# Performance work log

Hardware: AMD Instinct MI355X
Metric: run time of the kernel (lower is better)

## Reference

```python
import jax, jax.numpy as jnp
import numpy as np

CHUNK = 128
EPS = 1e-12


def causal_prod(q, k, v, chunk=CHUNK):
    """Chunk-parallel causal linear attention numerator and denominator.
    q,k: [B,H,S,D]; v: [B,H,S,E].
    Returns N: [B,H,S,E] = q_n . cumsum_{m<=n}(k_m v_m^T)
            D: [B,H,S]   = q_n . cumsum_{m<=n} k_m
    """
    B, H, S, D = q.shape
    E = v.shape[-1]
    nc = S // chunk
    # [nc, B, H, C, D]
    qc = q.reshape(B, H, nc, chunk, D).transpose(2, 0, 1, 3, 4)
    kc = k.reshape(B, H, nc, chunk, D).transpose(2, 0, 1, 3, 4)
    vc = v.reshape(B, H, nc, chunk, E).transpose(2, 0, 1, 3, 4)
    mask = jnp.tril(jnp.ones((chunk, chunk), dtype=bool))  # j <= i

    def step(carry, xs):
        S_state, Z_state = carry  # [B,H,D,E], [B,H,D]
        qb, kb, vb = xs           # [B,H,C,D], [B,H,C,D], [B,H,C,E]
        scores = jnp.einsum('bhid,bhjd->bhij', qb, kb)
        scores = jnp.where(mask, scores, 0.0)
        # intra-chunk causal part + inter-chunk state part
        Nb = jnp.einsum('bhij,bhje->bhie', scores, vb) \
             + jnp.einsum('bhid,bhde->bhie', qb, S_state)
        Db = scores.sum(-1) + jnp.einsum('bhid,bhd->bhi', qb, Z_state)
        S_state = S_state + jnp.einsum('bhjd,bhje->bhde', kb, vb)
        Z_state = Z_state + kb.sum(axis=2)
        return (S_state, Z_state), (Nb, Db)

    init = (jnp.zeros((B, H, D, E), q.dtype), jnp.zeros((B, H, D), q.dtype))
    _, (N, Dv) = jax.lax.scan(step, init, (qc, kc, vc))
    N = N.transpose(1, 2, 0, 3, 4).reshape(B, H, S, E)
    Dv = Dv.transpose(1, 2, 0, 3).reshape(B, H, S)
    return N, Dv


def setup_inputs() -> dict:
    key = jax.random.key(0)
    k0, k1, k2, k3, k4 = jax.random.split(key, 5)
    B, H, S, D = 2, 8, 4096, 64
    # feature-mapped q/k are positive (softmax random features) -> uniform
    q = jax.random.uniform(k0, (B, H, S, D), dtype=jnp.float32)
    k = jax.random.uniform(k1, (B, H, S, D), dtype=jnp.float32)
    q_rot = jax.random.uniform(k2, (B, H, S, D), dtype=jnp.float32)
    k_rot = jax.random.uniform(k3, (B, H, S, D), dtype=jnp.float32)
    v = jax.random.normal(k4, (B, H, S, D), dtype=jnp.float32)
    return {"q": q, "k": k, "q_rot": q_rot, "k_rot": k_rot, "v": v, "horizon": 512}


def reference(q, k, q_rot, k_rot, v, horizon):
    # causal_linear_attention with local=horizon, rotary branch active
    N1, D1 = causal_prod(q, k, v)
    N2, D2 = causal_prod(q_rot, k_rot, v)
    N = N1 + N2
    Dd = D1 + D2
    local = horizon
    # subtract contribution of keys older than the local window
    ql = q[:, :, local:]
    kl = k[:, :, :-local]
    vl = v[:, :, :-local]
    qrl = q_rot[:, :, local:]
    krl = k_rot[:, :, :-local]
    Ns1, Ds1 = causal_prod(ql, kl, vl)
    Ns2, Ds2 = causal_prod(qrl, krl, vl)
    N = N.at[:, :, local:].add(-(Ns1 + Ns2))
    Dd = Dd.at[:, :, local:].add(-(Ds1 + Ds2))
    out = N * (1.0 / (Dd + EPS))[..., None]
    return out
```

## Files before the change

### kernel.cpp

```cpp
#include <hip/hip_runtime.h>

#define S_LEN 4096
#define Dh 64
#define BQ 128
#define BK 64
#define THREADS 256

typedef __attribute__((ext_vector_type(8))) short bf16x8;
typedef __attribute__((ext_vector_type(4))) float f32x4;

__device__ __forceinline__ short f2bf(float f) {
    union { float f; unsigned u; } c; c.f = f;
    unsigned u = c.u + 0x7FFFu + ((c.u >> 16) & 1u);
    return (short)(u >> 16);
}

__global__ __launch_bounds__(THREADS, 2) void swin_attn(
    const float* __restrict__ q, const float* __restrict__ k,
    const float* __restrict__ qr, const float* __restrict__ kr,
    const float* __restrict__ v, const int* __restrict__ hor,
    float* __restrict__ out)
{
    const int W = hor[0];
    const int q0 = blockIdx.x * BQ;
    const int bh = blockIdx.y;
    const size_t base = (size_t)bh * S_LEN * Dh;

    const int tid = threadIdx.x;
    const int lane = tid & 63;
    const int wv = tid >> 6;
    const int g = lane >> 4;
    const int l16 = lane & 15;

    __shared__ __align__(16) char sK[BK * 256];
    __shared__ __align__(16) char sV[64 * 128];
    __shared__ __align__(16) char sS[4][32 * 128];

    bf16x8 qf[2][4];
    #pragma unroll
    for (int rb = 0; rb < 2; ++rb) {
        int qg = q0 + wv * 32 + rb * 16 + l16;
        const float* qrow  = q  + base + (size_t)qg * Dh;
        const float* qrrow = qr + base + (size_t)qg * Dh;
        #pragma unroll
        for (int fb = 0; fb < 4; ++fb) {
            int feat = fb * 32 + g * 8;
            const float* src = (feat < 64) ? (qrow + feat) : (qrrow + (feat - 64));
            f32x4 a = *(const f32x4*)src;
            f32x4 b = *(const f32x4*)(src + 4);
            bf16x8 fr;
            #pragma unroll
            for (int j = 0; j < 4; ++j) { fr[j] = f2bf(a[j]); fr[4 + j] = f2bf(b[j]); }
            qf[rb][fb] = fr;
        }
    }

    f32x4 nacc[2][4];
    f32x4 dacc[2];
    #pragma unroll
    for (int rb = 0; rb < 2; ++rb) {
        dacc[rb] = (f32x4){0.f, 0.f, 0.f, 0.f};
        #pragma unroll
        for (int eb = 0; eb < 4; ++eb) nacc[rb][eb] = (f32x4){0.f, 0.f, 0.f, 0.f};
    }
    bf16x8 ones;
    #pragma unroll
    for (int j = 0; j < 8; ++j) ones[j] = (short)0x3F80;

    const int lo_key = q0 - (W - 1);
    const int kt_lo = (lo_key <= 0) ? 0 : (lo_key >> 6);
    const int kt_hi = (q0 + BQ - 1) >> 6;

    for (int kt = kt_lo; kt <= kt_hi; ++kt) {
        const int k0 = kt << 6;
        __syncthreads();

        #pragma unroll
        for (int i = 0; i < 4; ++i) {
            int c = tid + THREADS * i;
            int row = c >> 4;
            int f0 = (c & 15) * 8;
            const float* src = (f0 < 64) ? (k  + base + (size_t)(k0 + row) * Dh + f0)
                                         : (kr + base + (size_t)(k0 + row) * Dh + (f0 - 64));
            f32x4 a = *(const f32x4*)src;
            f32x4 b = *(const f32x4*)(src + 4);
            bf16x8 w8;
            #pragma unroll
            for (int j = 0; j < 4; ++j) { w8[j] = f2bf(a[j]); w8[4 + j] = f2bf(b[j]); }
            int off = row * 256 + ((f0 * 2) ^ ((row & 7) << 4));
            *(bf16x8*)(sK + off) = w8;
        }
        #pragma unroll
        for (int i = 0; i < 4; ++i) {
            int c = tid + THREADS * i;
            int row = c >> 4;
            int c4 = (c & 15) * 4;
            f32x4 a = *(const f32x4*)(v + base + (size_t)(k0 + row) * Dh + c4);
            #pragma unroll
            for (int j = 0; j < 4; ++j) {
                int e = c4 + j;
                int off = e * 128 + ((row * 2) ^ ((e & 7) << 4));
                *(short*)(sV + off) = f2bf(a[j]);
            }
        }
        __syncthreads();

        const bool dense = (k0 + BK - 1 <= q0) && (k0 >= q0 + BQ - 1 - (W - 1));

        #pragma unroll
        for (int kb = 0; kb < 4; ++kb) {
            bf16x8 kf[4];
            const int key = kb * 16 + l16;
            const int rowoff = key * 256;
            const int sw = (key & 7) << 4;
            #pragma unroll
            for (int fb = 0; fb < 4; ++fb)
                kf[fb] = *(const bf16x8*)(sK + rowoff + ((fb * 64 + g * 16) ^ sw));
            #pragma unroll
            for (int rb = 0; rb < 2; ++rb) {
                f32x4 s = {0.f, 0.f, 0.f, 0.f};
                #pragma unroll
                for (int fb = 0; fb < 4; ++fb)
                    s = __builtin_amdgcn_mfma_f32_16x16x32_bf16(qf[rb][fb], kf[fb], s, 0, 0, 0);
                const int qrow0 = rb * 16 + g * 4;
                const int qg0 = q0 + wv * 32 + qrow0;
                const int mg = k0 + kb * 16 + l16;
                if (!dense) {
                    #pragma unroll
                    for (int r = 0; r < 4; ++r) {
                        unsigned d = (unsigned)(qg0 + r - mg);
                        if (d >= (unsigned)W) s[r] = 0.f;
                    }
                }
                #pragma unroll
                for (int r = 0; r < 4; ++r) {
                    int row = qrow0 + r;
                    int off = row * 128 + (((kb * 16 + l16) * 2) ^ ((row & 7) << 4));
                    *(short*)(sS[wv] + off) = f2bf(s[r]);
                }
            }
        }

        #pragma unroll
        for (int kb2 = 0; kb2 < 2; ++kb2) {
            bf16x8 af[2];
            #pragma unroll
            for (int rb = 0; rb < 2; ++rb) {
                int row = rb * 16 + l16;
                int off = row * 128 + ((kb2 * 64 + g * 16) ^ ((row & 7) << 4));
                af[rb] = *(const bf16x8*)(sS[wv] + off);
            }
            #pragma unroll
            for (int rb = 0; rb < 2; ++rb)
                dacc[rb] = __builtin_amdgcn_mfma_f32_16x16x32_bf16(af[rb], ones, dacc[rb], 0, 0, 0);
            #pragma unroll
            for (int eb = 0; eb < 4; ++eb) {
                int e = eb * 16 + l16;
                int off = e * 128 + ((kb2 * 64 + g * 16) ^ ((e & 7) << 4));
                bf16x8 bfr = *(const bf16x8*)(sV + off);
                #pragma unroll
                for (int rb = 0; rb < 2; ++rb)
                    nacc[rb][eb] = __builtin_amdgcn_mfma_f32_16x16x32_bf16(af[rb], bfr, nacc[rb][eb], 0, 0, 0);
            }
        }
    }

    #pragma unroll
    for (int rb = 0; rb < 2; ++rb) {
        f32x4 rc;
        #pragma unroll
        for (int r = 0; r < 4; ++r) rc[r] = 1.0f / (dacc[rb][r] + 1e-12f);
        const int qg0 = q0 + wv * 32 + rb * 16 + g * 4;
        #pragma unroll
        for (int eb = 0; eb < 4; ++eb) {
            #pragma unroll
            for (int r = 0; r < 4; ++r) {
                out[base + (size_t)(qg0 + r) * Dh + eb * 16 + l16] = nacc[rb][eb][r] * rc[r];
            }
        }
    }
}

extern "C" void kernel_launch(void* const* d_in, const int* in_sizes, int n_in,
                              void* d_out, int out_size, void* d_ws, size_t ws_size,
                              hipStream_t stream) {
    const float* q  = (const float*)d_in[0];
    const float* k  = (const float*)d_in[1];
    const float* qr = (const float*)d_in[2];
    const float* kr = (const float*)d_in[3];
    const float* v  = (const float*)d_in[4];
    const int* hor  = (const int*)d_in[5];
    float* out = (float*)d_out;

    const int BH = in_sizes[0] / (S_LEN * Dh);
    dim3 grid(S_LEN / BQ, BH);
    hipLaunchKernelGGL(swin_attn, grid, dim3(THREADS), 0, stream,
                       q, k, qr, kr, v, hor, out);
}
```

Measured before the change: 49.89 us.

## Halve query tile, remap grid for XCD locality, coalesce V staging

Shrinks the query block from 128 to 64 rows, with each wave handling 16 query rows instead of 32, and raises the launch-bounds occupancy hint to 4 blocks per CU. The grid becomes one-dimensional with an XCD-aware remap, so that neighbouring query tiles of the same head land on the same XCD and share K/V in its L2. The V transpose into shared memory now has each thread read four rows of one column and do a single 8-byte LDS store, instead of four 2-byte stores. The cost is twice as many blocks, so each K/V tile is loaded and converted more times in total, and there is less MFMA work per K-tile load.

```diff
diff --git a/kernel.cpp b/kernel.cpp
--- a/kernel.cpp
+++ b/kernel.cpp
@@ -2,12 +2,14 @@
 
 #define S_LEN 4096
 #define Dh 64
-#define BQ 128
+#define BQ 64
 #define BK 64
 #define THREADS 256
+#define NXCD 8
 
 typedef __attribute__((ext_vector_type(8))) short bf16x8;
 typedef __attribute__((ext_vector_type(4))) float f32x4;
+typedef __attribute__((ext_vector_type(4))) short bf16x4;
 
 __device__ __forceinline__ short f2bf(float f) {
     union { float f; unsigned u; } c; c.f = f;
@@ -15,15 +17,19 @@
     return (short)(u >> 16);
 }
 
-__global__ __launch_bounds__(THREADS, 2) void swin_attn(
+__global__ __launch_bounds__(THREADS, 4) void swin_attn(
     const float* __restrict__ q, const float* __restrict__ k,
     const float* __restrict__ qr, const float* __restrict__ kr,
     const float* __restrict__ v, const int* __restrict__ hor,
     float* __restrict__ out)
 {
     const int W = hor[0];
-    const int q0 = blockIdx.x * BQ;
-    const int bh = blockIdx.y;
+
+    const int nwg = gridDim.x;
+    const int cpx = nwg >> 3;
+    const int wg = (blockIdx.x & (NXCD - 1)) * cpx + (blockIdx.x >> 3);
+    const int bh = wg >> 6;
+    const int q0 = (wg & 63) * BQ;
     const size_t base = (size_t)bh * S_LEN * Dh;
 
     const int tid = threadIdx.x;
@@ -34,12 +40,11 @@
 
     __shared__ __align__(16) char sK[BK * 256];
     __shared__ __align__(16) char sV[64 * 128];
-    __shared__ __align__(16) char sS[4][32 * 128];
+    __shared__ __align__(16) char sS[4][16 * 128];
 
-    bf16x8 qf[2][4];
-    #pragma unroll
-    for (int rb = 0; rb < 2; ++rb) {
-        int qg = q0 + wv * 32 + rb * 16 + l16;
+    bf16x8 qf[4];
+    {
+        int qg = q0 + wv * 16 + l16;
         const float* qrow  = q  + base + (size_t)qg * Dh;
         const float* qrrow = qr + base + (size_t)qg * Dh;
         #pragma unroll
@@ -51,25 +56,21 @@
             bf16x8 fr;
             #pragma unroll
             for (int j = 0; j < 4; ++j) { fr[j] = f2bf(a[j]); fr[4 + j] = f2bf(b[j]); }
-            qf[rb][fb] = fr;
+            qf[fb] = fr;
         }
     }
 
-    f32x4 nacc[2][4];
-    f32x4 dacc[2];
+    f32x4 nacc[4];
+    f32x4 dacc = (f32x4){0.f, 0.f, 0.f, 0.f};
     #pragma unroll
-    for (int rb = 0; rb < 2; ++rb) {
-        dacc[rb] = (f32x4){0.f, 0.f, 0.f, 0.f};
-        #pragma unroll
-        for (int eb = 0; eb < 4; ++eb) nacc[rb][eb] = (f32x4){0.f, 0.f, 0.f, 0.f};
-    }
+    for (int eb = 0; eb < 4; ++eb) nacc[eb] = (f32x4){0.f, 0.f, 0.f, 0.f};
     bf16x8 ones;
     #pragma unroll
     for (int j = 0; j < 8; ++j) ones[j] = (short)0x3F80;
 
     const int lo_key = q0 - (W - 1);
     const int kt_lo = (lo_key <= 0) ? 0 : (lo_key >> 6);
-    const int kt_hi = (q0 + BQ - 1) >> 6;
+    const int kt_hi = q0 >> 6;
 
     for (int kt = kt_lo; kt <= kt_hi; ++kt) {
         const int k0 = kt << 6;
@@ -93,15 +94,17 @@
         #pragma unroll
         for (int i = 0; i < 4; ++i) {
             int c = tid + THREADS * i;
-            int row = c >> 4;
-            int c4 = (c & 15) * 4;
-            f32x4 a = *(const f32x4*)(v + base + (size_t)(k0 + row) * Dh + c4);
-            #pragma unroll
-            for (int j = 0; j < 4; ++j) {
-                int e = c4 + j;
-                int off = e * 128 + ((row * 2) ^ ((e & 7) << 4));
-                *(short*)(sV + off) = f2bf(a[j]);
-            }
+            int e = c & 63;
+            int k4 = c >> 6;
+            const float* src = v + base + (size_t)(k0 + k4 * 4) * Dh + e;
+            float a0 = src[0];
+            float a1 = src[Dh];
+            float a2 = src[2 * Dh];
+            float a3 = src[3 * Dh];
+            bf16x4 w4;
+            w4[0] = f2bf(a0); w4[1] = f2bf(a1); w4[2] = f2bf(a2); w4[3] = f2bf(a3);
+            int off = e * 128 + ((k4 * 8) ^ ((e & 7) << 4));
+            *(bf16x4*)(sV + off) = w4;
         }
         __syncthreads();
 
@@ -116,67 +119,53 @@
             #pragma unroll
             for (int fb = 0; fb < 4; ++fb)
                 kf[fb] = *(const bf16x8*)(sK + rowoff + ((fb * 64 + g * 16) ^ sw));
+            f32x4 s = {0.f, 0.f, 0.f, 0.f};
             #pragma unroll
-            for (int rb = 0; rb < 2; ++rb) {
-                f32x4 s = {0.f, 0.f, 0.f, 0.f};
-                #pragma unroll
-                for (int fb = 0; fb < 4; ++fb)
-                    s = __builtin_amdgcn_mfma_f32_16x16x32_bf16(qf[rb][fb], kf[fb], s, 0, 0, 0);
-                const int qrow0 = rb * 16 + g * 4;
-                const int qg0 = q0 + wv * 32 + qrow0;
-                const int mg = k0 + kb * 16 + l16;
-                if (!dense) {
-                    #pragma unroll
-                    for (int r = 0; r < 4; ++r) {
-                        unsigned d = (unsigned)(qg0 + r - mg);
-                        if (d >= (unsigned)W) s[r] = 0.f;
-                    }
-                }
+            for (int fb = 0; fb < 4; ++fb)
+                s = __builtin_amdgcn_mfma_f32_16x16x32_bf16(qf[fb], kf[fb], s, 0, 0, 0);
+            const int qrow0 = g * 4;
+            const int qg0 = q0 + wv * 16 + qrow0;
+            const int mg = k0 + kb * 16 + l16;
+            if (!dense) {
                 #pragma unroll
                 for (int r = 0; r < 4; ++r) {
-                    int row = qrow0 + r;
-                    int off = row * 128 + (((kb * 16 + l16) * 2) ^ ((row & 7) << 4));
-                    *(short*)(sS[wv] + off) = f2bf(s[r]);
+                    unsigned d = (unsigned)(qg0 + r - mg);
+                    if (d >= (unsigned)W) s[r] = 0.f;
                 }
+            }
+            #pragma unroll
+            for (int r = 0; r < 4; ++r) {
+                int row = qrow0 + r;
+                int off = row * 128 + (((kb * 16 + l16) * 2) ^ ((row & 7) << 4));
+                *(short*)(sS[wv] + off) = f2bf(s[r]);
             }
         }
 
         #pragma unroll
         for (int kb2 = 0; kb2 < 2; ++kb2) {
-            bf16x8 af[2];
-            #pragma unroll
-            for (int rb = 0; rb < 2; ++rb) {
-                int row = rb * 16 + l16;
-                int off = row * 128 + ((kb2 * 64 + g * 16) ^ ((row & 7) << 4));
-                af[rb] = *(const bf16x8*)(sS[wv] + off);
-            }
-            #pragma unroll
-            for (int rb = 0; rb < 2; ++rb)
-                dacc[rb] = __builtin_amdgcn_mfma_f32_16x16x32_bf16(af[rb], ones, dacc[rb], 0, 0, 0);
+            int arow = l16;
+            int aoff = arow * 128 + ((kb2 * 64 + g * 16) ^ ((arow & 7) << 4));
+            bf16x8 af = *(const bf16x8*)(sS[wv] + aoff);
+            dacc = __builtin_amdgcn_mfma_f32_16x16x32_bf16(af, ones, dacc, 0, 0, 0);
             #pragma unroll
             for (int eb = 0; eb < 4; ++eb) {
                 int e = eb * 16 + l16;
                 int off = e * 128 + ((kb2 * 64 + g * 16) ^ ((e & 7) << 4));
                 bf16x8 bfr = *(const bf16x8*)(sV + off);
-                #pragma unroll
-                for (int rb = 0; rb < 2; ++rb)
-                    nacc[rb][eb] = __builtin_amdgcn_mfma_f32_16x16x32_bf16(af[rb], bfr, nacc[rb][eb], 0, 0, 0);
+                nacc[eb] = __builtin_amdgcn_mfma_f32_16x16x32_bf16(af, bfr, nacc[eb], 0, 0, 0);
             }
         }
     }
 
+    f32x4 rc;
     #pragma unroll
-    for (int rb = 0; rb < 2; ++rb) {
-        f32x4 rc;
+    for (int r = 0; r < 4; ++r) rc[r] = 1.0f / (dacc[r] + 1e-12f);
+    const int qg0 = q0 + wv * 16 + g * 4;
+    #pragma unroll
+    for (int eb = 0; eb < 4; ++eb) {
         #pragma unroll
-        for (int r = 0; r < 4; ++r) rc[r] = 1.0f / (dacc[rb][r] + 1e-12f);
-        const int qg0 = q0 + wv * 32 + rb * 16 + g * 4;
-        #pragma unroll
-        for (int eb = 0; eb < 4; ++eb) {
-            #pragma unroll
-            for (int r = 0; r < 4; ++r) {
-                out[base + (size_t)(qg0 + r) * Dh + eb * 16 + l16] = nacc[rb][eb][r] * rc[r];
-            }
+        for (int r = 0; r < 4; ++r) {
+            out[base + (size_t)(qg0 + r) * Dh + eb * 16 + l16] = nacc[eb][r] * rc[r];
         }
     }
 }
@@ -193,7 +182,7 @@
     float* out = (float*)d_out;
 
     const int BH = in_sizes[0] / (S_LEN * Dh);
-    dim3 grid(S_LEN / BQ, BH);
+    dim3 grid((S_LEN / BQ) * BH);
     hipLaunchKernelGGL(swin_attn, grid, dim3(THREADS), 0, stream,
                        q, k, qr, kr, v, hor, out);
 }
```

After: 58.16 us. 16.6% more time.

## Prepack K/V to swizzled bf16 workspace and double-buffer via global_load_lds

Applied to the files above, without the earlier changes.

Adds a prepack kernel that converts K, K_rot and V once into bf16 tiles in the workspace, already swizzled and with V transposed, so each key tile is converted once instead of once per query block that reads it. The attention kernel then streams these tiles straight into LDS with global_load_lds, double-buffered so the next tile loads while the current one computes. It also remaps block IDs so neighbouring blocks run on related heads. The cost is an extra kernel launch and a workspace round trip. A fallback kernel with vectorised V transposition is used when the workspace is too small.

```diff
diff --git a/kernel.cpp b/kernel.cpp
--- a/kernel.cpp
+++ b/kernel.cpp
@@ -2,12 +2,15 @@
 
 #define S_LEN 4096
 #define Dh 64
-#define BQ 128
-#define BK 64
 #define THREADS 256
+#define KC_TILE 16384
+#define VT_TILE 8192
+#define VT_BASE 16777216ull
+#define WS_NEED 25165824ull
 
 typedef __attribute__((ext_vector_type(8))) short bf16x8;
 typedef __attribute__((ext_vector_type(4))) float f32x4;
+typedef __attribute__((ext_vector_type(4))) short bf16x4;
 
 __device__ __forceinline__ short f2bf(float f) {
     union { float f; unsigned u; } c; c.f = f;
@@ -15,15 +18,62 @@
     return (short)(u >> 16);
 }
 
-__global__ __launch_bounds__(THREADS, 2) void swin_attn(
-    const float* __restrict__ q, const float* __restrict__ k,
-    const float* __restrict__ qr, const float* __restrict__ kr,
-    const float* __restrict__ v, const int* __restrict__ hor,
+__device__ __forceinline__ void gload16(const void* g, void* l) {
+    __builtin_amdgcn_global_load_lds(
+        (const __attribute__((address_space(1))) unsigned int*)g,
+        (__attribute__((address_space(3))) unsigned int*)l, 16, 0, 0);
+}
+
+__global__ __launch_bounds__(THREADS) void prepack(
+    const float* __restrict__ k, const float* __restrict__ kr,
+    const float* __restrict__ v, char* __restrict__ ws)
+{
+    const int t = blockIdx.x * THREADS + threadIdx.x;
+    {
+        const int bh = t >> 16;
+        const int r1 = t & 65535;
+        const int tile = r1 >> 10;
+        const int r2 = r1 & 1023;
+        const int row = r2 >> 4;
+        const int f0 = (r2 & 15) * 8;
+        const size_t rbase = ((size_t)bh * S_LEN + tile * 64 + row) * Dh;
+        const float* src = (f0 < 64) ? (k + rbase + f0) : (kr + rbase + (f0 - 64));
+        f32x4 a = *(const f32x4*)src;
+        f32x4 b = *(const f32x4*)(src + 4);
+        bf16x8 w;
+        #pragma unroll
+        for (int j = 0; j < 4; ++j) { w[j] = f2bf(a[j]); w[4 + j] = f2bf(b[j]); }
+        const int off = row * 256 + ((f0 * 2) ^ ((row & 7) << 4));
+        *(bf16x8*)(ws + (size_t)(bh * 64 + tile) * KC_TILE + off) = w;
+    }
+    {
+        const int bh = t >> 16;
+        const int r1 = t & 65535;
+        const int tile = r1 >> 10;
+        const int r2 = r1 & 1023;
+        const int e = r2 & 63;
+        const int k4 = r2 >> 6;
+        const float* src = v + ((size_t)bh * S_LEN + tile * 64 + k4 * 4) * Dh + e;
+        bf16x4 w;
+        w[0] = f2bf(src[0]);
+        w[1] = f2bf(src[Dh]);
+        w[2] = f2bf(src[2 * Dh]);
+        w[3] = f2bf(src[3 * Dh]);
+        const int off = e * 128 + ((k4 * 8) ^ ((e & 7) << 4));
+        *(bf16x4*)(ws + VT_BASE + (size_t)(bh * 64 + tile) * VT_TILE + off) = w;
+    }
+}
+
+__global__ __launch_bounds__(THREADS, 2) void swin_attn2(
+    const float* __restrict__ q, const float* __restrict__ qr,
+    const char* __restrict__ ws, const int* __restrict__ hor,
     float* __restrict__ out)
 {
     const int W = hor[0];
-    const int q0 = blockIdx.x * BQ;
-    const int bh = blockIdx.y;
+    const int bid = blockIdx.x;
+    const int wg = (bid & 7) * 64 + (bid >> 3);
+    const int bh = wg >> 5;
+    const int q0 = (wg & 31) * 128;
     const size_t base = (size_t)bh * S_LEN * Dh;
 
     const int tid = threadIdx.x;
@@ -32,9 +82,9 @@
     const int g = lane >> 4;
     const int l16 = lane & 15;
 
-    __shared__ __align__(16) char sK[BK * 256];
-    __shared__ __align__(16) char sV[64 * 128];
-    __shared__ __align__(16) char sS[4][32 * 128];
+    __shared__ __align__(16) char sK[2][KC_TILE];
+    __shared__ __align__(16) char sV[2][VT_TILE];
+    __shared__ __align__(16) char sS[4][4096];
 
     bf16x8 qf[2][4];
     #pragma unroll
@@ -69,43 +119,45 @@
 
     const int lo_key = q0 - (W - 1);
     const int kt_lo = (lo_key <= 0) ? 0 : (lo_key >> 6);
-    const int kt_hi = (q0 + BQ - 1) >> 6;
-
+    const int kt_hi = (q0 + 127) >> 6;
+
+    const char* KcB = ws + (size_t)(bh << 6) * KC_TILE;
+    const char* VtB = ws + VT_BASE + (size_t)(bh << 6) * VT_TILE;
+
+    asm volatile("s_waitcnt vmcnt(0)" ::: "memory");
+    __builtin_amdgcn_sched_barrier(0);
+
+#define STAGE(B, KT)                                                              \
+    do {                                                                          \
+        const char* kg_ = KcB + (size_t)(KT) * KC_TILE + wv * 4096 + lane * 16;   \
+        const char* vg_ = VtB + (size_t)(KT) * VT_TILE + wv * 2048 + lane * 16;   \
+        _Pragma("unroll")                                                         \
+        for (int i_ = 0; i_ < 4; ++i_)                                            \
+            gload16(kg_ + i_ * 1024, &sK[B][wv * 4096 + i_ * 1024]);              \
+        _Pragma("unroll")                                                         \
+        for (int i_ = 0; i_ < 2; ++i_)                                            \
+            gload16(vg_ + i_ * 1024, &sV[B][wv * 2048 + i_ * 1024]);              \
+    } while (0)
+
+    STAGE(0, kt_lo);
+
+    int buf = 0;
     for (int kt = kt_lo; kt <= kt_hi; ++kt) {
         const int k0 = kt << 6;
-        __syncthreads();
-
-        #pragma unroll
-        for (int i = 0; i < 4; ++i) {
-            int c = tid + THREADS * i;
-            int row = c >> 4;
-            int f0 = (c & 15) * 8;
-            const float* src = (f0 < 64) ? (k  + base + (size_t)(k0 + row) * Dh + f0)
-                                         : (kr + base + (size_t)(k0 + row) * Dh + (f0 - 64));
-            f32x4 a = *(const f32x4*)src;
-            f32x4 b = *(const f32x4*)(src + 4);
-            bf16x8 w8;
-            #pragma unroll
-            for (int j = 0; j < 4; ++j) { w8[j] = f2bf(a[j]); w8[4 + j] = f2bf(b[j]); }
-            int off = row * 256 + ((f0 * 2) ^ ((row & 7) << 4));
-            *(bf16x8*)(sK + off) = w8;
-        }
-        #pragma unroll
-        for (int i = 0; i < 4; ++i) {
-            int c = tid + THREADS * i;
-            int row = c >> 4;
-            int c4 = (c & 15) * 4;
-            f32x4 a = *(const f32x4*)(v + base + (size_t)(k0 + row) * Dh + c4);
-            #pragma unroll
-            for (int j = 0; j < 4; ++j) {
-                int e = c4 + j;
-                int off = e * 128 + ((row * 2) ^ ((e & 7) << 4));
-                *(short*)(sV + off) = f2bf(a[j]);
-            }
-        }
-        __syncthreads();
-
-        const bool dense = (k0 + BK - 1 <= q0) && (k0 >= q0 + BQ - 1 - (W - 1));
+        const bool more = (kt < kt_hi);
+        if (more) {
+            STAGE(buf ^ 1, kt + 1);
+            asm volatile("s_waitcnt vmcnt(6)" ::: "memory");
+        } else {
+            asm volatile("s_waitcnt vmcnt(0)" ::: "memory");
+        }
+        __builtin_amdgcn_sched_barrier(0);
+        __builtin_amdgcn_s_barrier();
+        asm volatile("" ::: "memory");
+
+        const char* Kb = sK[buf];
+        const char* Vb = sV[buf];
+        const bool dense = (k0 + 63 <= q0) && (k0 >= q0 + 127 - (W - 1));
 
         #pragma unroll
         for (int kb = 0; kb < 4; ++kb) {
@@ -115,7 +167,7 @@
             const int sw = (key & 7) << 4;
             #pragma unroll
             for (int fb = 0; fb < 4; ++fb)
-                kf[fb] = *(const bf16x8*)(sK + rowoff + ((fb * 64 + g * 16) ^ sw));
+                kf[fb] = *(const bf16x8*)(Kb + rowoff + ((fb * 64 + g * 16) ^ sw));
             #pragma unroll
             for (int rb = 0; rb < 2; ++rb) {
                 f32x4 s = {0.f, 0.f, 0.f, 0.f};
@@ -157,6 +209,173 @@
             for (int eb = 0; eb < 4; ++eb) {
                 int e = eb * 16 + l16;
                 int off = e * 128 + ((kb2 * 64 + g * 16) ^ ((e & 7) << 4));
+                bf16x8 bfr = *(const bf16x8*)(Vb + off);
+                #pragma unroll
+                for (int rb = 0; rb < 2; ++rb)
+                    nacc[rb][eb] = __builtin_amdgcn_mfma_f32_16x16x32_bf16(af[rb], bfr, nacc[rb][eb], 0, 0, 0);
+            }
+        }
+
+        asm volatile("" ::: "memory");
+        __builtin_amdgcn_s_barrier();
+        buf ^= 1;
+    }
+#undef STAGE
+
+    #pragma unroll
+    for (int rb = 0; rb < 2; ++rb) {
+        f32x4 rc;
+        #pragma unroll
+        for (int r = 0; r < 4; ++r) rc[r] = 1.0f / (dacc[rb][r] + 1e-12f);
+        const int qg0 = q0 + wv * 32 + rb * 16 + g * 4;
+        #pragma unroll
+        for (int eb = 0; eb < 4; ++eb) {
+            #pragma unroll
+            for (int r = 0; r < 4; ++r) {
+                out[base + (size_t)(qg0 + r) * Dh + eb * 16 + l16] = nacc[rb][eb][r] * rc[r];
+            }
+        }
+    }
+}
+
+__global__ __launch_bounds__(THREADS, 2) void swin_attn_fb(
+    const float* __restrict__ q, const float* __restrict__ k,
+    const float* __restrict__ qr, const float* __restrict__ kr,
+    const float* __restrict__ v, const int* __restrict__ hor,
+    float* __restrict__ out)
+{
+    const int W = hor[0];
+    const int q0 = blockIdx.x * 128;
+    const int bh = blockIdx.y;
+    const size_t base = (size_t)bh * S_LEN * Dh;
+
+    const int tid = threadIdx.x;
+    const int lane = tid & 63;
+    const int wv = tid >> 6;
+    const int g = lane >> 4;
+    const int l16 = lane & 15;
+
+    __shared__ __align__(16) char sK[64 * 256];
+    __shared__ __align__(16) char sV[64 * 128];
+    __shared__ __align__(16) char sS[4][32 * 128];
+
+    bf16x8 qf[2][4];
+    #pragma unroll
+    for (int rb = 0; rb < 2; ++rb) {
+        int qg = q0 + wv * 32 + rb * 16 + l16;
+        const float* qrow  = q  + base + (size_t)qg * Dh;
+        const float* qrrow = qr + base + (size_t)qg * Dh;
+        #pragma unroll
+        for (int fb = 0; fb < 4; ++fb) {
+            int feat = fb * 32 + g * 8;
+            const float* src = (feat < 64) ? (qrow + feat) : (qrrow + (feat - 64));
+            f32x4 a = *(const f32x4*)src;
+            f32x4 b = *(const f32x4*)(src + 4);
+            bf16x8 fr;
+            #pragma unroll
+            for (int j = 0; j < 4; ++j) { fr[j] = f2bf(a[j]); fr[4 + j] = f2bf(b[j]); }
+            qf[rb][fb] = fr;
+        }
+    }
+
+    f32x4 nacc[2][4];
+    f32x4 dacc[2];
+    #pragma unroll
+    for (int rb = 0; rb < 2; ++rb) {
+        dacc[rb] = (f32x4){0.f, 0.f, 0.f, 0.f};
+        #pragma unroll
+        for (int eb = 0; eb < 4; ++eb) nacc[rb][eb] = (f32x4){0.f, 0.f, 0.f, 0.f};
+    }
+    bf16x8 ones;
+    #pragma unroll
+    for (int j = 0; j < 8; ++j) ones[j] = (short)0x3F80;
+
+    const int lo_key = q0 - (W - 1);
+    const int kt_lo = (lo_key <= 0) ? 0 : (lo_key >> 6);
+    const int kt_hi = (q0 + 127) >> 6;
+
+    for (int kt = kt_lo; kt <= kt_hi; ++kt) {
+        const int k0 = kt << 6;
+        __syncthreads();
+        #pragma unroll
+        for (int i = 0; i < 4; ++i) {
+            int c = tid + THREADS * i;
+            int row = c >> 4;
+            int f0 = (c & 15) * 8;
+            const float* src = (f0 < 64) ? (k  + base + (size_t)(k0 + row) * Dh + f0)
+                                         : (kr + base + (size_t)(k0 + row) * Dh + (f0 - 64));
+            f32x4 a = *(const f32x4*)src;
+            f32x4 b = *(const f32x4*)(src + 4);
+            bf16x8 w8;
+            #pragma unroll
+            for (int j = 0; j < 4; ++j) { w8[j] = f2bf(a[j]); w8[4 + j] = f2bf(b[j]); }
+            int off = row * 256 + ((f0 * 2) ^ ((row & 7) << 4));
+            *(bf16x8*)(sK + off) = w8;
+        }
+        #pragma unroll
+        for (int i = 0; i < 4; ++i) {
+            int c = tid + THREADS * i;
+            int e = c & 63;
+            int k4 = c >> 6;
+            const float* src = v + base + (size_t)(k0 + k4 * 4) * Dh + e;
+            bf16x4 w4;
+            w4[0] = f2bf(src[0]); w4[1] = f2bf(src[Dh]);
+            w4[2] = f2bf(src[2 * Dh]); w4[3] = f2bf(src[3 * Dh]);
+            int off = e * 128 + ((k4 * 8) ^ ((e & 7) << 4));
+            *(bf16x4*)(sV + off) = w4;
+        }
+        __syncthreads();
+
+        const bool dense = (k0 + 63 <= q0) && (k0 >= q0 + 127 - (W - 1));
+        #pragma unroll
+        for (int kb = 0; kb < 4; ++kb) {
+            bf16x8 kf[4];
+            const int key = kb * 16 + l16;
+            const int rowoff = key * 256;
+            const int sw = (key & 7) << 4;
+            #pragma unroll
+            for (int fb = 0; fb < 4; ++fb)
+                kf[fb] = *(const bf16x8*)(sK + rowoff + ((fb * 64 + g * 16) ^ sw));
+            #pragma unroll
+            for (int rb = 0; rb < 2; ++rb) {
+                f32x4 s = {0.f, 0.f, 0.f, 0.f};
+                #pragma unroll
+                for (int fb = 0; fb < 4; ++fb)
+                    s = __builtin_amdgcn_mfma_f32_16x16x32_bf16(qf[rb][fb], kf[fb], s, 0, 0, 0);
+                const int qrow0 = rb * 16 + g * 4;
+                const int qg0 = q0 + wv * 32 + qrow0;
+                const int mg = k0 + kb * 16 + l16;
+                if (!dense) {
+                    #pragma unroll
+                    for (int r = 0; r < 4; ++r) {
+                        unsigned d = (unsigned)(qg0 + r - mg);
+                        if (d >= (unsigned)W) s[r] = 0.f;
+                    }
+                }
+                #pragma unroll
+                for (int r = 0; r < 4; ++r) {
+                    int row = qrow0 + r;
+                    int off = row * 128 + (((kb * 16 + l16) * 2) ^ ((row & 7) << 4));
+                    *(short*)(sS[wv] + off) = f2bf(s[r]);
+                }
+            }
+        }
+        #pragma unroll
+        for (int kb2 = 0; kb2 < 2; ++kb2) {
+            bf16x8 af[2];
+            #pragma unroll
+            for (int rb = 0; rb < 2; ++rb) {
+                int row = rb * 16 + l16;
+                int off = row * 128 + ((kb2 * 64 + g * 16) ^ ((row & 7) << 4));
+                af[rb] = *(const bf16x8*)(sS[wv] + off);
+            }
+            #pragma unroll
+            for (int rb = 0; rb < 2; ++rb)
+                dacc[rb] = __builtin_amdgcn_mfma_f32_16x16x32_bf16(af[rb], ones, dacc[rb], 0, 0, 0);
+            #pragma unroll
+            for (int eb = 0; eb < 4; ++eb) {
+                int e = eb * 16 + l16;
+                int off = e * 128 + ((kb2 * 64 + g * 16) ^ ((e & 7) << 4));
                 bf16x8 bfr = *(const bf16x8*)(sV + off);
                 #pragma unroll
                 for (int rb = 0; rb < 2; ++rb)
@@ -191,9 +410,15 @@
     const float* v  = (const float*)d_in[4];
     const int* hor  = (const int*)d_in[5];
     float* out = (float*)d_out;
-
     const int BH = in_sizes[0] / (S_LEN * Dh);
-    dim3 grid(S_LEN / BQ, BH);
-    hipLaunchKernelGGL(swin_attn, grid, dim3(THREADS), 0, stream,
-                       q, k, qr, kr, v, hor, out);
-}
+
+    if (ws_size >= WS_NEED) {
+        hipLaunchKernelGGL(prepack, dim3(4096), dim3(THREADS), 0, stream,
+                           k, kr, v, (char*)d_ws);
+        hipLaunchKernelGGL(swin_attn2, dim3((S_LEN / 128) * BH), dim3(THREADS), 0, stream,
+                           q, qr, (const char*)d_ws, hor, out);
+    } else {
+        hipLaunchKernelGGL(swin_attn_fb, dim3(S_LEN / 128, BH), dim3(THREADS), 0, stream,
+                           q, k, qr, kr, v, hor, out);
+    }
+}
```

After: 52.66 us. 1.06x slower.
